# Performance work log

Measured on AMD Instinct MI355X. Metric: run time of the kernel, lower is better.

The kernel has to match this reference:

```python
import jax, jax.numpy as jnp
import numpy as np

B, L, D = 1, 2048, 1024
H, F, HD = 16, 16, 64  # heads, feature_dim, head_dim
EPS = 1e-12


def setup_inputs() -> dict:
    key = jax.random.key(0)
    k1, k2, k3, k4, k5 = jax.random.split(key, 5)
    s = lambda fan_in: 1.0 / np.sqrt(fan_in)
    return {
        "hidden_states": jax.random.normal(k1, (B, L, D), jnp.float32),
        "Wq": jax.random.normal(k2, (D, H * F), jnp.float32) * s(D),
        "Wk": jax.random.normal(k3, (D, H * F), jnp.float32) * s(D),
        "Wv": jax.random.normal(k4, (D, H * HD), jnp.float32) * s(D),
        "Wo": jax.random.normal(k5, (H * HD, D), jnp.float32) * s(H * HD),
    }


def reference(hidden_states, Wq, Wk, Wv, Wo):
    b, l, _ = hidden_states.shape
    # projections (nn.Linear, no bias); reshape to (b, h, l, d)
    q = (hidden_states @ Wq).reshape(b, l, H, F).transpose(0, 2, 1, 3)
    k = (hidden_states @ Wk).reshape(b, l, H, F).transpose(0, 2, 1, 3)
    v = (hidden_states @ Wv).reshape(b, l, H, HD).transpose(0, 2, 1, 3)
    # feature map is identity. Causal quadratic linear attention:
    A = jnp.einsum("bhnd,bhmd->bhnm", q, k)          # [b,h,l,l]
    A = jnp.tril(A)
    y = jnp.einsum("bhnm,bhme->bhne", A, v)          # [b,h,l,hd]
    # denominator: q . cumsum(k)
    z = 1.0 / (jnp.einsum("bhld,bhld->bhl", q, jnp.cumsum(k, axis=2)) + EPS)
    y = y * z[..., None]
    # merge heads and output projection
    y = y.transpose(0, 2, 1, 3).reshape(b, l, H * HD)
    return y @ Wo
```

## Files before the change

### kernel.cpp

```cpp
#include <hip/hip_runtime.h>

constexpr int L  = 2048;
constexpr int D  = 1024;
constexpr int H  = 16;
constexpr int F  = 16;
constexpr int HD = 64;
constexpr int CHUNK = 128;
constexpr int NC = L / CHUNK;

typedef __bf16 bf16x8 __attribute__((ext_vector_type(8)));
typedef float  f32x16 __attribute__((ext_vector_type(16)));
typedef int    i32x4  __attribute__((ext_vector_type(4)));

__device__ __forceinline__ ushort f2bf(float f) {
  uint u = __builtin_bit_cast(uint, f);
  uint r = (u + 0x7FFFu + ((u >> 16) & 1u)) >> 16;
  return (ushort)r;
}

__device__ __forceinline__ void split5(float x, signed char s[5]) {
  float t = rintf(x * 16.f);              s[0] = (signed char)t;
  float r = fmaf(t, -6.25e-2f, x);
  t = rintf(r * 2048.f);                  s[1] = (signed char)t;
  r = fmaf(t, -4.8828125e-4f, r);
  t = rintf(r * 262144.f);                s[2] = (signed char)t;
  r = fmaf(t, -3.814697265625e-6f, r);
  t = rintf(r * 33554432.f);              s[3] = (signed char)t;
  r = fmaf(t, -2.9802322387695312e-8f, r);
  t = rintf(r * 4294967296.f);            s[4] = (signed char)t;
}

__global__ __launch_bounds__(256) void split_hs_i8(
    const float* __restrict__ X, ushort* __restrict__ Ah, signed char* __restrict__ A8) {
  const int plane = L * D;
  int idx = blockIdx.x * 256 + threadIdx.x;
  if (idx >= plane / 4) return;
  float4 v = ((const float4*)X)[idx];
  ushort4 hh;
  hh.x = f2bf(v.x); hh.y = f2bf(v.y); hh.z = f2bf(v.z); hh.w = f2bf(v.w);
  ((ushort4*)Ah)[idx] = hh;
  signed char sx[5], sy[5], sz[5], sw[5];
  split5(v.x, sx); split5(v.y, sy); split5(v.z, sz); split5(v.w, sw);
  #pragma unroll
  for (int s = 0; s < 5; ++s) {
    char4 c; c.x = sx[s]; c.y = sy[s]; c.z = sz[s]; c.w = sw[s];
    ((char4*)(A8 + (size_t)s * plane))[idx] = c;
  }
}

__global__ __launch_bounds__(256) void wsplit_all(
    const float* __restrict__ Wv, const float* __restrict__ Wo,
    const float* __restrict__ Wq, const float* __restrict__ Wk,
    ushort* __restrict__ BvT, ushort* __restrict__ BoT, signed char* __restrict__ W8) {
  __shared__ float t[32][33];
  const int tid = threadIdx.x;
  const int lx = tid & 31, ly = tid >> 5;
  if (blockIdx.z == 2) {
    if (blockIdx.x >= 16) return;
    const int plane = 512 * 1024;
    const int bn = blockIdx.x * 32, bk = blockIdx.y * 32;
    const float* W = (bn < 256) ? Wq : Wk;
    const int wn = bn & 255;
    #pragma unroll
    for (int i = 0; i < 32; i += 8)
      t[ly + i][lx] = W[(size_t)(bk + ly + i) * 256 + wn + lx];
    __syncthreads();
    #pragma unroll
    for (int i = 0; i < 32; i += 8) {
      float v = t[lx][ly + i];
      signed char s[5];
      split5(v, s);
      size_t base = (size_t)(bn + ly + i) * 1024 + bk + lx;
      #pragma unroll
      for (int si = 0; si < 5; ++si) W8[(size_t)si * plane + base] = s[si];
    }
    return;
  }
  const float* W = blockIdx.z ? Wo : Wv;
  ushort* BT = blockIdx.z ? BoT : BvT;
  const int bn = blockIdx.x * 32, bk = blockIdx.y * 32;
  #pragma unroll
  for (int i = 0; i < 32; i += 8)
    t[ly + i][lx] = W[(size_t)(bk + ly + i) * 1024 + bn + lx];
  __syncthreads();
  #pragma unroll
  for (int i = 0; i < 32; i += 8) {
    float v = t[lx][ly + i];
    BT[(size_t)(bn + ly + i) * 1024 + bk + lx] = f2bf(v);
  }
}

__global__ __launch_bounds__(256) void gemm_bf16_db(
    const ushort* __restrict__ A, const ushort* __restrict__ BT,
    float* __restrict__ C, int M, int N, int K) {
  constexpr int LDT = 40;
  __shared__ __bf16 As[2][64][LDT];
  __shared__ __bf16 Bs[2][64][LDT];
  const int tid  = threadIdx.x;
  const int wave = tid >> 6, lane = tid & 63;
  const int wr = (wave >> 1) * 32, wc = (wave & 1) * 32;
  const int nbx = gridDim.x, nwg = gridDim.x * gridDim.y;
  int bid = blockIdx.y * nbx + blockIdx.x;
  bid = (bid & 7) * (nwg >> 3) + (bid >> 3);
  const int brow = (bid / nbx) * 64, bcol = (bid % nbx) * 64;
  const int srow = tid >> 2, skg = (tid & 3) * 8;
  const size_t a_off = (size_t)(brow + srow) * K + skg;
  const size_t b_off = (size_t)(bcol + srow) * K + skg;

  f32x16 acc;
  #pragma unroll
  for (int i = 0; i < 16; ++i) acc[i] = 0.f;

  bf16x8 ra, rb;
  auto LOADT = [&](int k0) {
    ra = *(const bf16x8*)&A[a_off + k0];
    rb = *(const bf16x8*)&BT[b_off + k0];
  };
  auto WRITET = [&](int buf) {
    *(bf16x8*)&As[buf][srow][skg] = ra;
    *(bf16x8*)&Bs[buf][srow][skg] = rb;
  };

  const int NS = K / 32;
  LOADT(0); WRITET(0);
  __syncthreads();
  int cur = 0;
  for (int t = 0; t < NS; ++t) {
    if (t + 1 < NS) LOADT((t + 1) * 32);
    const int fr = lane & 31;
    const int kh = (lane >> 5) * 8;
    bf16x8 a0 = *(const bf16x8*)&As[cur][wr + fr][kh];
    bf16x8 a1 = *(const bf16x8*)&As[cur][wr + fr][16 + kh];
    bf16x8 b0 = *(const bf16x8*)&Bs[cur][wc + fr][kh];
    bf16x8 b1 = *(const bf16x8*)&Bs[cur][wc + fr][16 + kh];
    acc = __builtin_amdgcn_mfma_f32_32x32x16_bf16(a0, b0, acc, 0, 0, 0);
    acc = __builtin_amdgcn_mfma_f32_32x32x16_bf16(a1, b1, acc, 0, 0, 0);
    if (t + 1 < NS) WRITET(cur ^ 1);
    __syncthreads();
    cur ^= 1;
  }
  const int fr = lane & 31, fq = lane >> 5;
  #pragma unroll
  for (int r = 0; r < 16; ++r) {
    int row = brow + wr + (r & 3) + 8 * (r >> 2) + 4 * fq;
    C[(size_t)row * N + bcol + wc + fr] = acc[r];
  }
}

__global__ __launch_bounds__(512) void gemm_qk_i8(
    const signed char* __restrict__ A8, const signed char* __restrict__ W8,
    float* __restrict__ Qo, float* __restrict__ Ko) {
  constexpr int LDT = 80;
  __shared__ signed char As[5][64][LDT];
  __shared__ signed char Bs[5][64][LDT];
  const int aplane = L * D;
  const int bplane = 512 * 1024;
  const int tid  = threadIdx.x;
  const int wave = tid >> 6, lane = tid & 63;
  const int wm = (wave >> 2) * 32;
  const int wn = (wave & 3) * 16;
  const int nbx = gridDim.x, nwg = gridDim.x * gridDim.y;
  int bid = blockIdx.y * nbx + blockIdx.x;
  bid = (bid & 7) * (nwg >> 3) + (bid >> 3);
  const int brow = (bid / nbx) * 64, bcol = (bid % nbx) * 64;
  const int fr = lane & 15, kq = (lane >> 4) * 16;

  i32x4 acc[2][5];
  #pragma unroll
  for (int fm = 0; fm < 2; ++fm)
    #pragma unroll
    for (int g = 0; g < 5; ++g)
      #pragma unroll
      for (int r = 0; r < 4; ++r) acc[fm][g][r] = 0;

  for (int k0 = 0; k0 < D; k0 += 64) {
    #pragma unroll
    for (int i = 0; i < 5; ++i) {
      int c = i * 512 + tid;
      int side = (c >= 1280);
      int cc = side ? c - 1280 : c;
      int slice = cc >> 8, row = (cc & 255) >> 2, c16 = (cc & 3) * 16;
      const signed char* src = side
          ? &W8[(size_t)slice * bplane + (size_t)(bcol + row) * 1024 + k0 + c16]
          : &A8[(size_t)slice * aplane + (size_t)(brow + row) * 1024 + k0 + c16];
      int4 val = *(const int4*)src;
      signed char* dst = side ? &Bs[slice][row][c16] : &As[slice][row][c16];
      *(int4*)dst = val;
    }
    __syncthreads();
    i32x4 bfr[5], afr[2][5];
    #pragma unroll
    for (int s = 0; s < 5; ++s) bfr[s] = *(const i32x4*)&Bs[s][wn + fr][kq];
    #pragma unroll
    for (int fm = 0; fm < 2; ++fm)
      #pragma unroll
      for (int s = 0; s < 5; ++s)
        afr[fm][s] = *(const i32x4*)&As[s][wm + fm * 16 + fr][kq];
    #pragma unroll
    for (int fm = 0; fm < 2; ++fm) {
      acc[fm][0] = __builtin_amdgcn_mfma_i32_16x16x64_i8(afr[fm][0], bfr[0], acc[fm][0], 0, 0, 0);
      #pragma unroll
      for (int g = 1; g < 5; ++g)
        #pragma unroll
        for (int i = 0; i <= g; ++i)
          acc[fm][g] = __builtin_amdgcn_mfma_i32_16x16x64_i8(afr[fm][i], bfr[g - i], acc[fm][g], 0, 0, 0);
    }
    __syncthreads();
  }
  const double sc0 = 3.90625e-3, sc1 = 3.0517578125e-5, sc2 = 2.384185791015625e-7,
               sc3 = 1.862645149230957e-9, sc4 = 1.4551915228366852e-11;
  float* Out = (bcol < 256) ? Qo : Ko;
  const int ocol = (bcol & 255) + wn + fr;
  #pragma unroll
  for (int fm = 0; fm < 2; ++fm)
    #pragma unroll
    for (int r = 0; r < 4; ++r) {
      double v = (double)acc[fm][0][r] * sc0 + (double)acc[fm][1][r] * sc1 +
                 (double)acc[fm][2][r] * sc2 + (double)acc[fm][3][r] * sc3 +
                 (double)acc[fm][4][r] * sc4;
      int row = brow + wm + fm * 16 + (lane >> 4) * 4 + r;
      Out[(size_t)row * 256 + ocol] = (float)v;
    }
}

__global__ __launch_bounds__(256) void chunk_state(
    const float* __restrict__ Kq, const float* __restrict__ V,
    float* __restrict__ S, double* __restrict__ KS) {
  const int c = blockIdx.x, h = blockIdx.y;
  __shared__ float Ks[CHUNK][F];
  __shared__ float Vs[CHUNK][HD];
  const int tid = threadIdx.x;
  #pragma unroll
  for (int i = 0; i < 2; ++i) {
    int g = i * 256 + tid;
    int m = g >> 2, f0 = (g & 3) * 4;
    *(float4*)&Ks[m][f0] = *(const float4*)&Kq[(size_t)(c * CHUNK + m) * (H * F) + h * F + f0];
  }
  #pragma unroll
  for (int i = 0; i < 8; ++i) {
    int g = i * 256 + tid;
    int m = g >> 4, e0 = (g & 15) * 4;
    *(float4*)&Vs[m][e0] = *(const float4*)&V[(size_t)(c * CHUNK + m) * (H * HD) + h * HD + e0];
  }
  __syncthreads();
  const int f = tid >> 4, e0 = (tid & 15) * 4;
  float4 acc = make_float4(0.f, 0.f, 0.f, 0.f);
  for (int m = 0; m < CHUNK; ++m) {
    float kv = Ks[m][f];
    float4 v4 = *(const float4*)&Vs[m][e0];
    acc.x = fmaf(kv, v4.x, acc.x);
    acc.y = fmaf(kv, v4.y, acc.y);
    acc.z = fmaf(kv, v4.z, acc.z);
    acc.w = fmaf(kv, v4.w, acc.w);
  }
  *(float4*)&S[((((size_t)h * NC) + c) * F + f) * HD + e0] = acc;
  if (tid < F) {
    double s = 0.0;
    for (int m = 0; m < CHUNK; ++m) s += (double)Ks[m][tid];
    KS[(((size_t)h * NC) + c) * F + tid] = s;
  }
}

__global__ __launch_bounds__(512) void attn_chunk_v4(
    const float* __restrict__ Q, const float* __restrict__ Kq, const float* __restrict__ V,
    const float* __restrict__ S, const double* __restrict__ KS,
    ushort* __restrict__ Yh) {
  const int c = blockIdx.x, h = blockIdx.y;
  __shared__ float Ks[CHUNK][F];
  __shared__ float Vs[CHUNK][HD];
  __shared__ float Ss[F][HD];
  __shared__ double kcs[F];
  __shared__ float zs[CHUNK];
  const int tid = threadIdx.x;

  {
    int m = tid >> 2, f0 = (tid & 3) * 4;
    *(float4*)&Ks[m][f0] = *(const float4*)&Kq[(size_t)(c * CHUNK + m) * (H * F) + h * F + f0];
  }
  #pragma unroll
  for (int i = 0; i < 4; ++i) {
    int g = i * 512 + tid;
    int m = g >> 4, e0 = (g & 15) * 4;
    *(float4*)&Vs[m][e0] = *(const float4*)&V[(size_t)(c * CHUNK + m) * (H * HD) + h * HD + e0];
  }
  {
    float s0 = 0.f, s1 = 0.f;
    for (int cc = 0; cc < c; ++cc) {
      size_t base = (((size_t)h * NC) + cc) * (F * HD);
      s0 += S[base + tid];
      s1 += S[base + tid + 512];
    }
    ((float*)Ss)[tid] = s0;
    ((float*)Ss)[tid + 512] = s1;
  }
  if (tid < F) {
    double rk = 0.0;
    for (int cc = 0; cc < c; ++cc) rk += KS[(((size_t)h * NC) + cc) * F + tid];
    kcs[tid] = rk;
  }
  __syncthreads();

  const int w = tid >> 6;
  const int lane = tid & 63;
  const int rsub = lane >> 3;
  const int cg = lane & 7;
  const int e0 = cg * 8;
  const int lr = 8 * w + rsub;
  const int hr = 120 - 8 * w + rsub;

  float ql[F], qh[F];
  #pragma unroll
  for (int f0 = 0; f0 < F; f0 += 4) {
    *(float4*)&ql[f0] = *(const float4*)&Q[(size_t)(c * CHUNK + lr) * (H * F) + h * F + f0];
    *(float4*)&qh[f0] = *(const float4*)&Q[(size_t)(c * CHUNK + hr) * (H * F) + h * F + f0];
  }

  float accl[8], acch[8];
  #pragma unroll
  for (int j = 0; j < 8; ++j) { accl[j] = 0.f; acch[j] = 0.f; }
  float denl = 0.f, denh = 0.f;

  const int m1 = 8 * w + 8;
  const int m2 = 128 - 8 * w;
  for (int m = 0; m < m2; ++m) {
    float kr[F];
    #pragma unroll
    for (int f0 = 0; f0 < F; f0 += 4)
      *(float4*)&kr[f0] = *(const float4*)&Ks[m][f0];
    float v8[8];
    *(float4*)&v8[0] = *(const float4*)&Vs[m][e0];
    *(float4*)&v8[4] = *(const float4*)&Vs[m][e0 + 4];
    {
      float s = 0.f;
      #pragma unroll
      for (int f = 0; f < F; ++f) s = fmaf(qh[f], kr[f], s);
      float a = (m <= hr) ? s : 0.f;
      denh += a;
      #pragma unroll
      for (int j = 0; j < 8; ++j) acch[j] = fmaf(a, v8[j], acch[j]);
    }
    if (m < m1) {
      float s = 0.f;
      #pragma unroll
      for (int f = 0; f < F; ++f) s = fmaf(ql[f], kr[f], s);
      float a = (m <= lr) ? s : 0.f;
      denl += a;
      #pragma unroll
      for (int j = 0; j < 8; ++j) accl[j] = fmaf(a, v8[j], accl[j]);
    }
  }

  #pragma unroll
  for (int f = 0; f < F; ++f) {
    float s8[8];
    *(float4*)&s8[0] = *(const float4*)&Ss[f][e0];
    *(float4*)&s8[4] = *(const float4*)&Ss[f][e0 + 4];
    #pragma unroll
    for (int j = 0; j < 8; ++j) {
      accl[j] = fmaf(ql[f], s8[j], accl[j]);
      acch[j] = fmaf(qh[f], s8[j], acch[j]);
    }
  }

  if (cg == 0) {
    double dl = (double)denl, dh = (double)denh;
    #pragma unroll
    for (int f = 0; f < F; ++f) {
      dl += (double)ql[f] * kcs[f];
      dh += (double)qh[f] * kcs[f];
    }
    zs[lr] = (float)(1.0 / (dl + 1e-12));
    zs[hr] = (float)(1.0 / (dh + 1e-12));
  }
  __syncthreads();

  #pragma unroll
  for (int rr = 0; rr < 2; ++rr) {
    const int row = rr ? hr : lr;
    const float* ac = rr ? acch : accl;
    float zz = zs[row];
    ushort4 h4a, h4b;
    h4a.x = f2bf(ac[0] * zz); h4a.y = f2bf(ac[1] * zz);
    h4a.z = f2bf(ac[2] * zz); h4a.w = f2bf(ac[3] * zz);
    h4b.x = f2bf(ac[4] * zz); h4b.y = f2bf(ac[5] * zz);
    h4b.z = f2bf(ac[6] * zz); h4b.w = f2bf(ac[7] * zz);
    size_t base = (size_t)(c * CHUNK + row) * 1024 + h * HD + e0;
    *(ushort4*)&Yh[base]     = h4a;
    *(ushort4*)&Yh[base + 4] = h4b;
  }
}

extern "C" void kernel_launch(void* const* d_in, const int* in_sizes, int n_in,
                              void* d_out, int out_size, void* d_ws, size_t ws_size,
                              hipStream_t stream) {
  const float* hs = (const float*)d_in[0];
  const float* Wq = (const float*)d_in[1];
  const float* Wk = (const float*)d_in[2];
  const float* Wv = (const float*)d_in[3];
  const float* Wo = (const float*)d_in[4];
  float* out = (float*)d_out;

  char* ws = (char*)d_ws;
  const size_t MB = 1 << 20;
  signed char* A8 = (signed char*)(ws + 0 * MB);
  signed char* W8 = (signed char*)(ws + 10 * MB);
  ushort* Ah  = (ushort*)(ws + 13 * MB);
  ushort* BvT = (ushort*)(ws + 17 * MB);
  ushort* BoT = (ushort*)(ws + 19 * MB);
  float*  Vb  = (float*)(ws + 21 * MB);
  float*  Qb  = (float*)(ws + 29 * MB);
  float*  S   = (float*)(ws + 13 * MB);
  ushort* Ys  = (ushort*)(ws + 0 * MB);
  double* KS  = (double*)d_out;
  float*  Kb  = (float*)((char*)d_out + 1 * MB);

  split_hs_i8<<<dim3(L * D / 4 / 256), 256, 0, stream>>>(hs, Ah, A8);
  wsplit_all<<<dim3(32, 32, 3), 256, 0, stream>>>(Wv, Wo, Wq, Wk, BvT, BoT, W8);
  gemm_bf16_db<<<dim3(16, 32), 256, 0, stream>>>(Ah, BvT, Vb, L, 1024, D);
  gemm_qk_i8<<<dim3(8, 32), 512, 0, stream>>>(A8, W8, Qb, Kb);
  chunk_state<<<dim3(NC, H), 256, 0, stream>>>(Kb, Vb, S, KS);
  attn_chunk_v4<<<dim3(NC, H), 512, 0, stream>>>(Qb, Kb, Vb, S, KS, Ys);
  gemm_bf16_db<<<dim3(16, 32), 256, 0, stream>>>(Ys, BoT, out, L, D, H * HD);
}
```

Measured before the change: 103.9 us.

## Merge prep kernels and run V and QK projection GEMMs in one launch

Folds the hidden-state split and weight split/transpose kernels into one prep launch with a flat block index. The int8 QK projection GEMM and the bf16 V projection GEMM now share one 512-thread launch, dispatched by block id. The V path moves to 128x64 tiles with 8 waves. This removes two launches and the serialization gaps between them, and lets the two GEMMs fill the GPU concurrently. The cost is a shared LDS allocation sized for the larger path, which may limit occupancy for the V blocks.

```diff
diff --git a/kernel.cpp b/kernel.cpp
--- a/kernel.cpp
+++ b/kernel.cpp
@@ -30,35 +30,39 @@
   t = rintf(r * 4294967296.f);            s[4] = (signed char)t;
 }
 
-__global__ __launch_bounds__(256) void split_hs_i8(
-    const float* __restrict__ X, ushort* __restrict__ Ah, signed char* __restrict__ A8) {
-  const int plane = L * D;
-  int idx = blockIdx.x * 256 + threadIdx.x;
-  if (idx >= plane / 4) return;
-  float4 v = ((const float4*)X)[idx];
-  ushort4 hh;
-  hh.x = f2bf(v.x); hh.y = f2bf(v.y); hh.z = f2bf(v.z); hh.w = f2bf(v.w);
-  ((ushort4*)Ah)[idx] = hh;
-  signed char sx[5], sy[5], sz[5], sw[5];
-  split5(v.x, sx); split5(v.y, sy); split5(v.z, sz); split5(v.w, sw);
-  #pragma unroll
-  for (int s = 0; s < 5; ++s) {
-    char4 c; c.x = sx[s]; c.y = sy[s]; c.z = sz[s]; c.w = sw[s];
-    ((char4*)(A8 + (size_t)s * plane))[idx] = c;
-  }
-}
-
-__global__ __launch_bounds__(256) void wsplit_all(
+__global__ __launch_bounds__(256) void prep_all(
+    const float* __restrict__ X,
     const float* __restrict__ Wv, const float* __restrict__ Wo,
     const float* __restrict__ Wq, const float* __restrict__ Wk,
+    ushort* __restrict__ Ah, signed char* __restrict__ A8,
     ushort* __restrict__ BvT, ushort* __restrict__ BoT, signed char* __restrict__ W8) {
   __shared__ float t[32][33];
   const int tid = threadIdx.x;
+  const int b = blockIdx.x;
+  if (b < 2048) {
+    const int plane = L * D;
+    int idx = b * 256 + tid;
+    float4 v = ((const float4*)X)[idx];
+    ushort4 hh;
+    hh.x = f2bf(v.x); hh.y = f2bf(v.y); hh.z = f2bf(v.z); hh.w = f2bf(v.w);
+    ((ushort4*)Ah)[idx] = hh;
+    signed char sx[5], sy[5], sz[5], sw[5];
+    split5(v.x, sx); split5(v.y, sy); split5(v.z, sz); split5(v.w, sw);
+    #pragma unroll
+    for (int s = 0; s < 5; ++s) {
+      char4 c; c.x = sx[s]; c.y = sy[s]; c.z = sz[s]; c.w = sw[s];
+      ((char4*)(A8 + (size_t)s * plane))[idx] = c;
+    }
+    return;
+  }
+  const int bb = b - 2048;
+  const int z = bb >> 10;
+  const int bx = (bb & 1023) & 31, by = (bb & 1023) >> 5;
   const int lx = tid & 31, ly = tid >> 5;
-  if (blockIdx.z == 2) {
-    if (blockIdx.x >= 16) return;
+  if (z == 2) {
+    if (bx >= 16) return;
     const int plane = 512 * 1024;
-    const int bn = blockIdx.x * 32, bk = blockIdx.y * 32;
+    const int bn = bx * 32, bk = by * 32;
     const float* W = (bn < 256) ? Wq : Wk;
     const int wn = bn & 255;
     #pragma unroll
@@ -76,9 +80,9 @@
     }
     return;
   }
-  const float* W = blockIdx.z ? Wo : Wv;
-  ushort* BT = blockIdx.z ? BoT : BvT;
-  const int bn = blockIdx.x * 32, bk = blockIdx.y * 32;
+  const float* W = z ? Wo : Wv;
+  ushort* BT = z ? BoT : BvT;
+  const int bn = bx * 32, bk = by * 32;
   #pragma unroll
   for (int i = 0; i < 32; i += 8)
     t[ly + i][lx] = W[(size_t)(bk + ly + i) * 1024 + bn + lx];
@@ -87,6 +91,136 @@
   for (int i = 0; i < 32; i += 8) {
     float v = t[lx][ly + i];
     BT[(size_t)(bn + ly + i) * 1024 + bk + lx] = f2bf(v);
+  }
+}
+
+__global__ __launch_bounds__(512) void gemm_v_qk(
+    const signed char* __restrict__ A8, const signed char* __restrict__ W8,
+    float* __restrict__ Qo, float* __restrict__ Ko,
+    const ushort* __restrict__ Av, const ushort* __restrict__ BvT,
+    float* __restrict__ Vb) {
+  __shared__ __align__(16) char lds_raw[51200];
+  const int tid = threadIdx.x;
+  const int bid = blockIdx.x;
+  const int wave = tid >> 6, lane = tid & 63;
+
+  if (bid < 256) {
+    auto As = (signed char (*)[64][80])(lds_raw);
+    auto Bs = (signed char (*)[64][80])(lds_raw + 25600);
+    const int aplane = L * D;
+    const int bplane = 512 * 1024;
+    const int wm = (wave >> 2) * 32;
+    const int wn = (wave & 3) * 16;
+    int b2 = (bid & 7) * 32 + (bid >> 3);
+    const int brow = (b2 >> 3) * 64, bcol = (b2 & 7) * 64;
+    const int fr = lane & 15, kq = (lane >> 4) * 16;
+
+    i32x4 acc[2][5];
+    #pragma unroll
+    for (int fm = 0; fm < 2; ++fm)
+      #pragma unroll
+      for (int g = 0; g < 5; ++g)
+        #pragma unroll
+        for (int r = 0; r < 4; ++r) acc[fm][g][r] = 0;
+
+    for (int k0 = 0; k0 < D; k0 += 64) {
+      #pragma unroll
+      for (int i = 0; i < 5; ++i) {
+        int c = i * 512 + tid;
+        int side = (c >= 1280);
+        int cc = side ? c - 1280 : c;
+        int slice = cc >> 8, row = (cc & 255) >> 2, c16 = (cc & 3) * 16;
+        const signed char* src = side
+            ? &W8[(size_t)slice * bplane + (size_t)(bcol + row) * 1024 + k0 + c16]
+            : &A8[(size_t)slice * aplane + (size_t)(brow + row) * 1024 + k0 + c16];
+        int4 val = *(const int4*)src;
+        signed char* dst = side ? &Bs[slice][row][c16] : &As[slice][row][c16];
+        *(int4*)dst = val;
+      }
+      __syncthreads();
+      i32x4 bfr[5], afr[2][5];
+      #pragma unroll
+      for (int s = 0; s < 5; ++s) bfr[s] = *(const i32x4*)&Bs[s][wn + fr][kq];
+      #pragma unroll
+      for (int fm = 0; fm < 2; ++fm)
+        #pragma unroll
+        for (int s = 0; s < 5; ++s)
+          afr[fm][s] = *(const i32x4*)&As[s][wm + fm * 16 + fr][kq];
+      #pragma unroll
+      for (int fm = 0; fm < 2; ++fm) {
+        acc[fm][0] = __builtin_amdgcn_mfma_i32_16x16x64_i8(afr[fm][0], bfr[0], acc[fm][0], 0, 0, 0);
+        #pragma unroll
+        for (int g = 1; g < 5; ++g)
+          #pragma unroll
+          for (int i = 0; i <= g; ++i)
+            acc[fm][g] = __builtin_amdgcn_mfma_i32_16x16x64_i8(afr[fm][i], bfr[g - i], acc[fm][g], 0, 0, 0);
+      }
+      __syncthreads();
+    }
+    const double sc0 = 3.90625e-3, sc1 = 3.0517578125e-5, sc2 = 2.384185791015625e-7,
+                 sc3 = 1.862645149230957e-9, sc4 = 1.4551915228366852e-11;
+    float* Out = (bcol < 256) ? Qo : Ko;
+    const int ocol = (bcol & 255) + wn + fr;
+    #pragma unroll
+    for (int fm = 0; fm < 2; ++fm)
+      #pragma unroll
+      for (int r = 0; r < 4; ++r) {
+        double v = (double)acc[fm][0][r] * sc0 + (double)acc[fm][1][r] * sc1 +
+                   (double)acc[fm][2][r] * sc2 + (double)acc[fm][3][r] * sc3 +
+                   (double)acc[fm][4][r] * sc4;
+        int row = brow + wm + fm * 16 + (lane >> 4) * 4 + r;
+        Out[(size_t)row * 256 + ocol] = (float)v;
+      }
+    return;
+  }
+
+  auto AsV = (__bf16 (*)[128][40])(lds_raw);
+  auto BsV = (__bf16 (*)[64][40])(lds_raw + 20480);
+  const int vb0 = bid - 256;
+  const int v2 = (vb0 & 7) * 32 + (vb0 >> 3);
+  const int brow = (v2 >> 4) * 128, bcol = (v2 & 15) * 64;
+  const int wm = (wave >> 1) * 32, wn = (wave & 1) * 32;
+  const int srow = tid >> 2, skg = (tid & 3) * 8;
+  const size_t a_off = (size_t)(brow + srow) * D + skg;
+  const size_t b_off = (size_t)(bcol + (tid >> 2)) * D + skg;
+
+  f32x16 acc;
+  #pragma unroll
+  for (int i = 0; i < 16; ++i) acc[i] = 0.f;
+
+  bf16x8 ra, rb;
+  auto LOADT = [&](int k0) {
+    ra = *(const bf16x8*)&Av[a_off + k0];
+    if (tid < 256) rb = *(const bf16x8*)&BvT[b_off + k0];
+  };
+  auto WRITET = [&](int buf) {
+    *(bf16x8*)&AsV[buf][srow][skg] = ra;
+    if (tid < 256) *(bf16x8*)&BsV[buf][tid >> 2][skg] = rb;
+  };
+
+  const int NS = D / 32;
+  LOADT(0); WRITET(0);
+  __syncthreads();
+  int cur = 0;
+  for (int t = 0; t < NS; ++t) {
+    if (t + 1 < NS) LOADT((t + 1) * 32);
+    const int fr = lane & 31;
+    const int kh = (lane >> 5) * 8;
+    bf16x8 a0 = *(const bf16x8*)&AsV[cur][wm + fr][kh];
+    bf16x8 a1 = *(const bf16x8*)&AsV[cur][wm + fr][16 + kh];
+    bf16x8 b0 = *(const bf16x8*)&BsV[cur][wn + fr][kh];
+    bf16x8 b1 = *(const bf16x8*)&BsV[cur][wn + fr][16 + kh];
+    acc = __builtin_amdgcn_mfma_f32_32x32x16_bf16(a0, b0, acc, 0, 0, 0);
+    acc = __builtin_amdgcn_mfma_f32_32x32x16_bf16(a1, b1, acc, 0, 0, 0);
+    if (t + 1 < NS) WRITET(cur ^ 1);
+    __syncthreads();
+    cur ^= 1;
+  }
+  const int fr = lane & 31, fq = lane >> 5;
+  #pragma unroll
+  for (int r = 0; r < 16; ++r) {
+    int row = brow + wm + (r & 3) + 8 * (r >> 2) + 4 * fq;
+    Vb[(size_t)row * 1024 + bcol + wn + fr] = acc[r];
   }
 }
 
@@ -147,82 +281,6 @@
   }
 }
 
-__global__ __launch_bounds__(512) void gemm_qk_i8(
-    const signed char* __restrict__ A8, const signed char* __restrict__ W8,
-    float* __restrict__ Qo, float* __restrict__ Ko) {
-  constexpr int LDT = 80;
-  __shared__ signed char As[5][64][LDT];
-  __shared__ signed char Bs[5][64][LDT];
-  const int aplane = L * D;
-  const int bplane = 512 * 1024;
-  const int tid  = threadIdx.x;
-  const int wave = tid >> 6, lane = tid & 63;
-  const int wm = (wave >> 2) * 32;
-  const int wn = (wave & 3) * 16;
-  const int nbx = gridDim.x, nwg = gridDim.x * gridDim.y;
-  int bid = blockIdx.y * nbx + blockIdx.x;
-  bid = (bid & 7) * (nwg >> 3) + (bid >> 3);
-  const int brow = (bid / nbx) * 64, bcol = (bid % nbx) * 64;
-  const int fr = lane & 15, kq = (lane >> 4) * 16;
-
-  i32x4 acc[2][5];
-  #pragma unroll
-  for (int fm = 0; fm < 2; ++fm)
-    #pragma unroll
-    for (int g = 0; g < 5; ++g)
-      #pragma unroll
-      for (int r = 0; r < 4; ++r) acc[fm][g][r] = 0;
-
-  for (int k0 = 0; k0 < D; k0 += 64) {
-    #pragma unroll
-    for (int i = 0; i < 5; ++i) {
-      int c = i * 512 + tid;
-      int side = (c >= 1280);
-      int cc = side ? c - 1280 : c;
-      int slice = cc >> 8, row = (cc & 255) >> 2, c16 = (cc & 3) * 16;
-      const signed char* src = side
-          ? &W8[(size_t)slice * bplane + (size_t)(bcol + row) * 1024 + k0 + c16]
-          : &A8[(size_t)slice * aplane + (size_t)(brow + row) * 1024 + k0 + c16];
-      int4 val = *(const int4*)src;
-      signed char* dst = side ? &Bs[slice][row][c16] : &As[slice][row][c16];
-      *(int4*)dst = val;
-    }
-    __syncthreads();
-    i32x4 bfr[5], afr[2][5];
-    #pragma unroll
-    for (int s = 0; s < 5; ++s) bfr[s] = *(const i32x4*)&Bs[s][wn + fr][kq];
-    #pragma unroll
-    for (int fm = 0; fm < 2; ++fm)
-      #pragma unroll
-      for (int s = 0; s < 5; ++s)
-        afr[fm][s] = *(const i32x4*)&As[s][wm + fm * 16 + fr][kq];
-    #pragma unroll
-    for (int fm = 0; fm < 2; ++fm) {
-      acc[fm][0] = __builtin_amdgcn_mfma_i32_16x16x64_i8(afr[fm][0], bfr[0], acc[fm][0], 0, 0, 0);
-      #pragma unroll
-      for (int g = 1; g < 5; ++g)
-        #pragma unroll
-        for (int i = 0; i <= g; ++i)
-          acc[fm][g] = __builtin_amdgcn_mfma_i32_16x16x64_i8(afr[fm][i], bfr[g - i], acc[fm][g], 0, 0, 0);
-    }
-    __syncthreads();
-  }
-  const double sc0 = 3.90625e-3, sc1 = 3.0517578125e-5, sc2 = 2.384185791015625e-7,
-               sc3 = 1.862645149230957e-9, sc4 = 1.4551915228366852e-11;
-  float* Out = (bcol < 256) ? Qo : Ko;
-  const int ocol = (bcol & 255) + wn + fr;
-  #pragma unroll
-  for (int fm = 0; fm < 2; ++fm)
-    #pragma unroll
-    for (int r = 0; r < 4; ++r) {
-      double v = (double)acc[fm][0][r] * sc0 + (double)acc[fm][1][r] * sc1 +
-                 (double)acc[fm][2][r] * sc2 + (double)acc[fm][3][r] * sc3 +
-                 (double)acc[fm][4][r] * sc4;
-      int row = brow + wm + fm * 16 + (lane >> 4) * 4 + r;
-      Out[(size_t)row * 256 + ocol] = (float)v;
-    }
-}
-
 __global__ __launch_bounds__(256) void chunk_state(
     const float* __restrict__ Kq, const float* __restrict__ V,
     float* __restrict__ S, double* __restrict__ KS) {
@@ -414,10 +472,8 @@
   double* KS  = (double*)d_out;
   float*  Kb  = (float*)((char*)d_out + 1 * MB);
 
-  split_hs_i8<<<dim3(L * D / 4 / 256), 256, 0, stream>>>(hs, Ah, A8);
-  wsplit_all<<<dim3(32, 32, 3), 256, 0, stream>>>(Wv, Wo, Wq, Wk, BvT, BoT, W8);
-  gemm_bf16_db<<<dim3(16, 32), 256, 0, stream>>>(Ah, BvT, Vb, L, 1024, D);
-  gemm_qk_i8<<<dim3(8, 32), 512, 0, stream>>>(A8, W8, Qb, Kb);
+  prep_all<<<dim3(5120), 256, 0, stream>>>(hs, Wv, Wo, Wq, Wk, Ah, A8, BvT, BoT, W8);
+  gemm_v_qk<<<dim3(512), 512, 0, stream>>>(A8, W8, Qb, Kb, Ah, BvT, Vb);
   chunk_state<<<dim3(NC, H), 256, 0, stream>>>(Kb, Vb, S, KS);
   attn_chunk_v4<<<dim3(NC, H), 512, 0, stream>>>(Qb, Kb, Vb, S, KS, Ys);
   gemm_bf16_db<<<dim3(16, 32), 256, 0, stream>>>(Ys, BoT, out, L, D, H * HD);
```

Measured after the change: 91.27 us. 12.1% less time.
